# Kernel optimization log

Hardware: AMD Instinct MI355X
Metric: run time of the kernel (lower is better)

Reference implementation:

```python
import jax, jax.numpy as jnp
import numpy as np

NQ = 6; DM = 128; CH = 4; SEQ = 2048; CHUNK = 16; BATCH = 128
NFP = 5 * NQ * 2   # feature params for 2 layers
NMP = 5 * NQ * 2   # mixing params for 2 layers

# ---- batched gate matrices (theta: (B,)) ----

def _rx(t):
    c = jnp.cos(t / 2).astype(jnp.complex64)
    s = (-1j * jnp.sin(t / 2)).astype(jnp.complex64)
    return jnp.stack([jnp.stack([c, s], -1), jnp.stack([s, c], -1)], -2)

def _ry(t):
    c = jnp.cos(t / 2).astype(jnp.complex64)
    s = jnp.sin(t / 2).astype(jnp.complex64)
    return jnp.stack([jnp.stack([c, -s], -1), jnp.stack([s, c], -1)], -2)

def _rz(t):
    e = jnp.exp(-1j * t.astype(jnp.complex64) / 2)
    z = jnp.zeros_like(e)
    return jnp.stack([jnp.stack([e, z], -1), jnp.stack([z, jnp.conj(e)], -1)], -2)

def _crx(t):
    B = t.shape[0]
    r = _rx(t)
    I = jnp.broadcast_to(jnp.eye(2, dtype=jnp.complex64), (B, 2, 2))
    Z = jnp.zeros((B, 2, 2), jnp.complex64)
    return jnp.concatenate([jnp.concatenate([I, Z], -1), jnp.concatenate([Z, r], -1)], -2)

# ---- batched statevector gate application; state: (B, 2, ..., 2) with axis 1+w = wire w ----

def _ap1(s, U, w):
    s = jnp.moveaxis(s, 1 + w, 1)
    sh = s.shape
    s = jnp.einsum('bij,bjr->bir', U, s.reshape(sh[0], 2, -1)).reshape(sh)
    return jnp.moveaxis(s, 1, 1 + w)

def _ap2(s, U, w0, w1):
    s = jnp.moveaxis(s, (1 + w0, 1 + w1), (1, 2))
    sh = s.shape
    s = jnp.einsum('bij,bjr->bir', U, s.reshape(sh[0], 4, -1)).reshape(sh)
    return jnp.moveaxis(s, (1, 2), (1 + w0, 1 + w1))

def _ansatz(s, p, off):
    # RX,RY,RZ on each qubit, then forward CRX ring, then backward CRX ring
    for i in range(NQ):
        s = _ap1(s, _rx(p[:, off + 3 * i]), i)
        s = _ap1(s, _ry(p[:, off + 3 * i + 1]), i)
        s = _ap1(s, _rz(p[:, off + 3 * i + 2]), i)
    off += 3 * NQ
    for i in range(NQ):
        s = _ap2(s, _crx(p[:, off]), i, (i + 1) % NQ)
        off += 1
    for i in range(NQ - 1, -1, -1):
        s = _ap2(s, _crx(p[:, off]), i, (i - 1) % NQ)
        off += 1
    return s, off

def _circuit(angles, fp, mp):
    B = angles.shape[0]
    s = jnp.zeros((B, 2 ** NQ), jnp.complex64).at[:, 0].set(1.0).reshape((B,) + (2,) * NQ)
    for i in range(NQ):                      # RY input embedding
        s = _ap1(s, _ry(angles[:, i]), i)
    off = 0
    for _ in range(2):                        # feature layers
        s, off = _ansatz(s, fp, off)
    off = 0
    for _ in range(2):                        # mixing layers
        s, off = _ansatz(s, mp, off)
    xs, ys, zs = [], [], []
    for i in range(NQ):                       # <X_i>, <Y_i>, <Z_i>
        v = jnp.moveaxis(s, 1 + i, 1).reshape(B, 2, -1)
        a, b = v[:, 0], v[:, 1]
        ab = jnp.sum(jnp.conj(a) * b, -1)
        xs.append(2 * jnp.real(ab))
        ys.append(2 * jnp.imag(ab))
        zs.append(jnp.sum(jnp.abs(a) ** 2 - jnp.abs(b) ** 2, -1))
    return jnp.stack(xs + ys + zs, 1)         # (B, 18) ordered X..Y..Z

def _ln(x, g, b, eps=1e-5):
    m = x.mean(-1, keepdims=True)
    v = ((x - m) ** 2).mean(-1, keepdims=True)
    return (x - m) / jnp.sqrt(v + eps) * g + b

def _fwd(x, conv_w, conv_b, ln1_g, ln1_b, ca1_w, ca1_b, ca2_w, ca2_b, pp_w, pp_b,
         ep_w, ep_b, op_w, op_b, ln2_g, ln2_b, sa1_w, sa1_b, sa2_w, sa2_b,
         cl1_w, cl1_b, cl2_w, cl2_b):
    B, C, S = x.shape
    h = jax.lax.conv_general_dilated(x, conv_w, (1,), [(1, 1)],
                                     dimension_numbers=('NCH', 'OIH', 'NCH')) + conv_b[None, :, None]
    h = jnp.transpose(h, (0, 2, 1))           # (B, S, D)
    h = _ln(h, ln1_g, ln1_b)
    nchunks = S // CHUNK
    h = h.reshape(B * nchunks, CHUNK, DM)
    sc = jnp.tanh(h @ ca1_w + ca1_b) @ ca2_w + ca2_b
    w = jax.nn.softmax(sc, axis=1)
    summ = jnp.sum(w * h, axis=1)             # (B*nchunks, D)
    ap = summ @ pp_w + pp_b
    fp, mp = ap[:, :NFP], ap[:, NFP:]
    ang = jnp.tanh(summ @ ep_w + ep_b) * np.pi
    q = _circuit(ang, fp, mp)                 # (B*nchunks, 18)
    cf = jax.nn.silu(_ln(q @ op_w + op_b, ln2_g, ln2_b))  # dropout = eval identity
    cf = cf.reshape(B, nchunks, DM)
    ss = jnp.tanh(cf @ sa1_w + sa1_b) @ sa2_w + sa2_b
    sw = jax.nn.softmax(ss, axis=1)
    rep = jnp.sum(sw * cf, axis=1)
    return jax.nn.silu(rep @ cl1_w + cl1_b) @ cl2_w + cl2_b

def setup_inputs() -> dict:
    key = jax.random.key(0)
    ks = jax.random.split(key, 16)
    n = lambda k, sh: (jax.random.normal(k, sh, jnp.float32) * 0.05)
    return {
        'x': jax.random.normal(ks[0], (BATCH, CH, SEQ), jnp.float32),
        'conv_w': n(ks[1], (DM, CH, 3)), 'conv_b': jnp.zeros((DM,), jnp.float32),
        'ln1_g': jnp.ones((DM,), jnp.float32), 'ln1_b': jnp.zeros((DM,), jnp.float32),
        'ca1_w': n(ks[2], (DM, DM // 4)), 'ca1_b': jnp.zeros((DM // 4,), jnp.float32),
        'ca2_w': n(ks[3], (DM // 4, 1)), 'ca2_b': jnp.zeros((1,), jnp.float32),
        'pp_w': n(ks[4], (DM, NFP + NMP)), 'pp_b': jnp.zeros((NFP + NMP,), jnp.float32),
        'ep_w': n(ks[5], (DM, NQ)), 'ep_b': jnp.zeros((NQ,), jnp.float32),
        'op_w': n(ks[6], (3 * NQ, DM)), 'op_b': jnp.zeros((DM,), jnp.float32),
        'ln2_g': jnp.ones((DM,), jnp.float32), 'ln2_b': jnp.zeros((DM,), jnp.float32),
        'sa1_w': n(ks[7], (DM, DM // 4)), 'sa1_b': jnp.zeros((DM // 4,), jnp.float32),
        'sa2_w': n(ks[8], (DM // 4, 1)), 'sa2_b': jnp.zeros((1,), jnp.float32),
        'cl1_w': n(ks[9], (DM, DM // 2)), 'cl1_b': jnp.zeros((DM // 2,), jnp.float32),
        'cl2_w': n(ks[10], (DM // 2, 2)), 'cl2_b': jnp.zeros((2,), jnp.float32),
    }

def reference(x, conv_w, conv_b, ln1_g, ln1_b, ca1_w, ca1_b, ca2_w, ca2_b, pp_w, pp_b,
              ep_w, ep_b, op_w, op_b, ln2_g, ln2_b, sa1_w, sa1_b, sa2_w, sa2_b,
              cl1_w, cl1_b, cl2_w, cl2_b):
    return _fwd(x, conv_w, conv_b, ln1_g, ln1_b, ca1_w, ca1_b, ca2_w, ca2_b, pp_w, pp_b,
                ep_w, ep_b, op_w, op_b, ln2_g, ln2_b, sa1_w, sa1_b, sa2_w, sa2_b,
                cl1_w, cl1_b, cl2_w, cl2_b)
```

## Files before the change

kernel.cpp:

```cpp
#include <hip/hip_runtime.h>
#include <math.h>


constexpr int kNQ    = 6;
constexpr int kDM    = 128;
constexpr int kCH    = 4;
constexpr int kSEQ   = 2048;
constexpr int kCHUNK = 16;
constexpr int kBATCH = 128;
constexpr int kNCH   = kSEQ / kCHUNK;
constexpr int kNP    = 120;
constexpr float kPI  = 3.14159265358979323846f;

typedef __attribute__((ext_vector_type(8))) short bf16x8;
typedef __attribute__((ext_vector_type(4))) float f32x4;

__device__ __forceinline__ float fast_tanh(float x) {
  float e = __expf(-2.f * fabsf(x));
  float r = (1.f - e) * __builtin_amdgcn_rcpf(1.f + e);
  return copysignf(r, x);
}
__device__ __forceinline__ float fast_silu(float x) {
  return x * __builtin_amdgcn_rcpf(1.f + __expf(-x));
}

template <int XM>
__device__ __forceinline__ float qp(float v) {
  constexpr int ctrl = (XM == 1) ? 0xB1 : 0x4E;
  return __int_as_float(
      __builtin_amdgcn_update_dpp(0, __float_as_int(v), ctrl, 0xF, 0xF, true));
}


template <int RB>
__device__ __forceinline__ void rx_reg(float c, float s, float* sr, float* si) {
#pragma unroll
  for (int r0 = 0; r0 < 16; ++r0) {
    if (r0 & RB) continue;
    int r1 = r0 | RB;
    float ar = sr[r0], ai = si[r0], br = sr[r1], bi = si[r1];
    sr[r0] = fmaf(c, ar,  s * bi);  si[r0] = fmaf(c, ai, -s * br);
    sr[r1] = fmaf(c, br,  s * ai);  si[r1] = fmaf(c, bi, -s * ar);
  }
}

template <int RB>
__device__ __forceinline__ void ry_reg(float c, float s, float* sr, float* si) {
#pragma unroll
  for (int r0 = 0; r0 < 16; ++r0) {
    if (r0 & RB) continue;
    int r1 = r0 | RB;
    float ar = sr[r0], ai = si[r0], br = sr[r1], bi = si[r1];
    sr[r0] = fmaf(c, ar, -s * br);  si[r0] = fmaf(c, ai, -s * bi);
    sr[r1] = fmaf(s, ar,  c * br);  si[r1] = fmaf(s, ai,  c * bi);
  }
}

template <int RB>
__device__ __forceinline__ void rz_reg(float c, float s, float* sr, float* si) {
#pragma unroll
  for (int r = 0; r < 16; ++r) {
    float sp = (r & RB) ? s : -s;
    float ar = sr[r], ai = si[r];
    sr[r] = fmaf(c, ar, -sp * ai);
    si[r] = fmaf(c, ai,  sp * ar);
  }
}

template <int XM>
__device__ __forceinline__ void rx_lane(float c, float s, float* sr, float* si) {
#pragma unroll
  for (int r = 0; r < 16; ++r) {
    float pr = qp<XM>(sr[r]), pi = qp<XM>(si[r]);
    sr[r] = fmaf(c, sr[r],  s * pi);
    si[r] = fmaf(c, si[r], -s * pr);
  }
}

template <int XM>
__device__ __forceinline__ void ry_lane(float c, float sg, float* sr, float* si) {
#pragma unroll
  for (int r = 0; r < 16; ++r) {
    float pr = qp<XM>(sr[r]), pi = qp<XM>(si[r]);
    sr[r] = fmaf(c, sr[r], sg * pr);
    si[r] = fmaf(c, si[r], sg * pi);
  }
}

__device__ __forceinline__ void rz_lane(float c, float sp, float* sr, float* si) {
#pragma unroll
  for (int r = 0; r < 16; ++r) {
    float ar = sr[r], ai = si[r];
    sr[r] = fmaf(c, ar, -sp * ai);
    si[r] = fmaf(c, ai,  sp * ar);
  }
}

template <int RB, int CB>
__device__ __forceinline__ void crx_reg_reg(float c, float s, float* sr, float* si) {
#pragma unroll
  for (int r0 = 0; r0 < 16; ++r0) {
    if ((r0 & RB) || !(r0 & CB)) continue;
    int r1 = r0 | RB;
    float ar = sr[r0], ai = si[r0], br = sr[r1], bi = si[r1];
    sr[r0] = fmaf(c, ar,  s * bi);  si[r0] = fmaf(c, ai, -s * br);
    sr[r1] = fmaf(c, br,  s * ai);  si[r1] = fmaf(c, bi, -s * ar);
  }
}

template <int XM, int CB>
__device__ __forceinline__ void crx_reg_lane(float c, float s, float* sr, float* si) {
#pragma unroll
  for (int r = 0; r < 16; ++r) {
    if (!(r & CB)) continue;
    float pr = qp<XM>(sr[r]), pi = qp<XM>(si[r]);
    sr[r] = fmaf(c, sr[r],  s * pi);
    si[r] = fmaf(c, si[r], -s * pr);
  }
}

template <int RB>
__device__ __forceinline__ void meas_reg(const float* sr, const float* si,
                                         float& tr, float& ti, float& zz) {
  tr = 0.f; ti = 0.f; zz = 0.f;
#pragma unroll
  for (int r0 = 0; r0 < 16; ++r0) {
    float n = fmaf(sr[r0], sr[r0], si[r0] * si[r0]);
    zz += (r0 & RB) ? -n : n;
    if (r0 & RB) continue;
    int r1 = r0 | RB;
    tr = fmaf(sr[r0], sr[r1], fmaf(si[r0], si[r1], tr));
    ti = fmaf(sr[r0], si[r1], fmaf(-si[r0], sr[r1], ti));
  }
  tr += qp<1>(tr); tr += qp<2>(tr);
  ti += qp<1>(ti); ti += qp<2>(ti);
  zz += qp<1>(zz); zz += qp<2>(zz);
}


__global__ __launch_bounds__(128) void k_pre(
    const float* __restrict__ x,
    const float* __restrict__ conv_w, const float* __restrict__ conv_b,
    const float* __restrict__ ln1_g,  const float* __restrict__ ln1_b,
    const float* __restrict__ ca1_w,  const float* __restrict__ ca1_b,
    const float* __restrict__ ca2_w,  const float* __restrict__ ca2_b,
    const float* __restrict__ pp_w,   const float* __restrict__ pp_b,
    const float* __restrict__ ep_w,   const float* __restrict__ ep_b,
    float* __restrict__ outb, int emit_cs)
{
  __shared__ float hbuf[kCHUNK][132];
  __shared__ __align__(16) float spart[2][16];
  __shared__ __align__(16) float summ[kDM];
  __shared__ float mrow[kCHUNK], irow[kCHUNK];

  const int tid   = threadIdx.x;
  const int chunk = blockIdx.x;
  const int b     = chunk >> 7;
  const int nc    = chunk & 127;
  const int t0    = nc * kCHUNK;
  const int d     = tid;
  const int lane  = tid & 63;
  const int wv    = tid >> 6;
  const int col   = (lane & 15) + 16 * wv;
  const int qd    = lane >> 4;

  float w12[12];
  {
    const float4* cw = (const float4*)(conv_w + d * 12);
    float4 a0 = cw[0], a1 = cw[1], a2 = cw[2];
    w12[0]=a0.x; w12[1]=a0.y; w12[2]=a0.z; w12[3]=a0.w;
    w12[4]=a1.x; w12[5]=a1.y; w12[6]=a1.z; w12[7]=a1.w;
    w12[8]=a2.x; w12[9]=a2.y; w12[10]=a2.z; w12[11]=a2.w;
  }
  float cb = conv_b[d];
  float g1 = ln1_g[d], b1 = ln1_b[d];
  float Bf[32];
#pragma unroll
  for (int ks = 0; ks < 4; ++ks)
#pragma unroll
    for (int jj = 0; jj < 8; ++jj)
      Bf[ks * 8 + jj] = ca1_w[(ks * 32 + qd * 8 + jj) * 32 + col];
  float cb1 = ca1_b[col], cw2 = ca2_w[col], cb2 = ca2_b[0];

  float h[kCHUNK];
#pragma unroll
  for (int t = 0; t < kCHUNK; ++t) h[t] = cb;
#pragma unroll
  for (int ch = 0; ch < kCH; ++ch) {
    const float* xb = x + ((size_t)b * kCH + ch) * kSEQ + t0 - 4;
    float xv[24];
#pragma unroll
    for (int sl = 1; sl <= 4; ++sl) {
      float4 v = *(const float4*)(xb + sl * 4);
      xv[sl*4+0]=v.x; xv[sl*4+1]=v.y; xv[sl*4+2]=v.z; xv[sl*4+3]=v.w;
    }
    if (nc > 0) {
      float4 v = *(const float4*)(xb);
      xv[0]=v.x; xv[1]=v.y; xv[2]=v.z; xv[3]=v.w;
    } else { xv[0]=xv[1]=xv[2]=xv[3]=0.f; }
    if (nc < 127) {
      float4 v = *(const float4*)(xb + 20);
      xv[20]=v.x; xv[21]=v.y; xv[22]=v.z; xv[23]=v.w;
    } else { xv[20]=xv[21]=xv[22]=xv[23]=0.f; }
    float c0 = w12[ch*3+0], c1 = w12[ch*3+1], c2 = w12[ch*3+2];
#pragma unroll
    for (int t = 0; t < kCHUNK; ++t)
      h[t] = fmaf(xv[t+3], c0, fmaf(xv[t+4], c1, fmaf(xv[t+5], c2, h[t])));
  }
#pragma unroll
  for (int t = 0; t < kCHUNK; ++t) hbuf[t][d] = h[t];
  __syncthreads();

  {
    int row = tid >> 3, k = tid & 7;
    const float4* rp = (const float4*)&hbuf[row][k * 16];
    float s1 = 0.f, s2 = 0.f;
#pragma unroll
    for (int q = 0; q < 4; ++q) {
      float4 v = rp[q];
      s1 += v.x + v.y + v.z + v.w;
      s2 = fmaf(v.x,v.x,s2); s2 = fmaf(v.y,v.y,s2);
      s2 = fmaf(v.z,v.z,s2); s2 = fmaf(v.w,v.w,s2);
    }
#pragma unroll
    for (int o = 1; o < 8; o <<= 1) {
      s1 += __shfl_xor(s1, o, 64);
      s2 += __shfl_xor(s2, o, 64);
    }
    if (k == 0) {
      float m = s1 * (1.f / kDM);
      mrow[row] = m;
      irow[row] = rsqrtf(s2 * (1.f / kDM) - m * m + 1e-5f);
    }
  }
  __syncthreads();

#pragma unroll
  for (int t = 0; t < kCHUNK; ++t) {
    h[t] = fmaf((h[t] - mrow[t]) * irow[t], g1, b1);
    unsigned hb = __float_as_uint(h[t]);
    float lof = h[t] - __uint_as_float(hb & 0xffff0000u);
    unsigned pk = (hb >> 16) | (__float_as_uint(lof) & 0xffff0000u);
    ((unsigned*)&hbuf[t][0])[d] = pk;
  }
  __syncthreads();

  bf16x8 bhi[4], blo[4];
#pragma unroll
  for (int ks = 0; ks < 4; ++ks)
#pragma unroll
    for (int jj = 0; jj < 8; ++jj) {
      float bvf = Bf[ks * 8 + jj];
      unsigned bb = __float_as_uint(bvf);
      bhi[ks][jj] = (short)(bb >> 16);
      float lf = bvf - __uint_as_float(bb & 0xffff0000u);
      blo[ks][jj] = (short)(__float_as_uint(lf) >> 16);
    }

  f32x4 acc = {0.f, 0.f, 0.f, 0.f};
  {
    const unsigned* hrow = (const unsigned*)&hbuf[lane & 15][0];
#pragma unroll
    for (int ks = 0; ks < 4; ++ks) {
      const uint4* ap = (const uint4*)(hrow + ks * 32 + qd * 8);
      uint4 w0 = ap[0], w1 = ap[1];
      bf16x8 ahi, alo;
      ahi[0] = (short)(w0.x & 0xffff); ahi[1] = (short)(w0.y & 0xffff);
      ahi[2] = (short)(w0.z & 0xffff); ahi[3] = (short)(w0.w & 0xffff);
      ahi[4] = (short)(w1.x & 0xffff); ahi[5] = (short)(w1.y & 0xffff);
      ahi[6] = (short)(w1.z & 0xffff); ahi[7] = (short)(w1.w & 0xffff);
      alo[0] = (short)(w0.x >> 16); alo[1] = (short)(w0.y >> 16);
      alo[2] = (short)(w0.z >> 16); alo[3] = (short)(w0.w >> 16);
      alo[4] = (short)(w1.x >> 16); alo[5] = (short)(w1.y >> 16);
      alo[6] = (short)(w1.z >> 16); alo[7] = (short)(w1.w >> 16);
      acc = __builtin_amdgcn_mfma_f32_16x16x32_bf16(ahi, bhi[ks], acc, 0, 0, 0);
      acc = __builtin_amdgcn_mfma_f32_16x16x32_bf16(ahi, blo[ks], acc, 0, 0, 0);
      acc = __builtin_amdgcn_mfma_f32_16x16x32_bf16(alo, bhi[ks], acc, 0, 0, 0);
    }
  }

  {
    float ev[4];
#pragma unroll
    for (int r = 0; r < 4; ++r)
      ev[r] = fast_tanh(acc[r] + cb1) * cw2;
#pragma unroll
    for (int o = 1; o < 16; o <<= 1)
#pragma unroll
      for (int r = 0; r < 4; ++r) ev[r] += __shfl_xor(ev[r], o, 64);
    if ((lane & 15) == 0)
      *(float4*)&spart[wv][qd * 4] = make_float4(ev[0], ev[1], ev[2], ev[3]);
  }
  __syncthreads();

  {
    float scl16[kCHUNK];
    const float4* s0 = (const float4*)&spart[0][0];
    const float4* s1 = (const float4*)&spart[1][0];
    float mx = -1e30f;
#pragma unroll
    for (int g = 0; g < 4; ++g) {
      float4 a = s0[g], bq = s1[g];
      scl16[g*4+0] = a.x + bq.x + cb2;
      scl16[g*4+1] = a.y + bq.y + cb2;
      scl16[g*4+2] = a.z + bq.z + cb2;
      scl16[g*4+3] = a.w + bq.w + cb2;
    }
#pragma unroll
    for (int t = 0; t < kCHUNK; ++t) mx = fmaxf(mx, scl16[t]);
    float e[kCHUNK], ssum = 0.f;
#pragma unroll
    for (int t = 0; t < kCHUNK; ++t) { e[t] = __expf(scl16[t] - mx); ssum += e[t]; }
    float inv = 1.f / ssum;
    float acc2 = 0.f;
#pragma unroll
    for (int t = 0; t < kCHUNK; ++t) acc2 = fmaf(e[t] * inv, h[t], acc2);
    summ[d] = acc2;
  }
  __syncthreads();

  if (tid < kNP) {
    float acc = pp_b[tid];
    const float4* s4 = (const float4*)summ;
#pragma unroll 8
    for (int q = 0; q < 32; ++q) {
      float4 v = s4[q];
      acc = fmaf(v.x, pp_w[(q*4+0)*kNP + tid], acc);
      acc = fmaf(v.y, pp_w[(q*4+1)*kNP + tid], acc);
      acc = fmaf(v.z, pp_w[(q*4+2)*kNP + tid], acc);
      acc = fmaf(v.w, pp_w[(q*4+3)*kNP + tid], acc);
    }
    float ha = 0.5f * acc;
    if (emit_cs) {
      ((float2*)(outb + (size_t)chunk * 256))[6 + tid] =
          make_float2(__cosf(ha), __sinf(ha));
    } else {
      outb[(size_t)chunk * 126 + 6 + tid] = ha;
    }
  } else if (tid < kNP + kNQ) {
    int jj = tid - kNP;
    float acc = ep_b[jj];
    const float4* s4 = (const float4*)summ;
#pragma unroll 8
    for (int q = 0; q < 32; ++q) {
      float4 v = s4[q];
      acc = fmaf(v.x, ep_w[(q*4+0)*kNQ + jj], acc);
      acc = fmaf(v.y, ep_w[(q*4+1)*kNQ + jj], acc);
      acc = fmaf(v.z, ep_w[(q*4+2)*kNQ + jj], acc);
      acc = fmaf(v.w, ep_w[(q*4+3)*kNQ + jj], acc);
    }
    float ha = 0.5f * fast_tanh(acc) * kPI;
    if (emit_cs) {
      ((float2*)(outb + (size_t)chunk * 256))[jj] =
          make_float2(__cosf(ha), __sinf(ha));
    } else {
      outb[(size_t)chunk * 126 + jj] = ha;
    }
  }
}


constexpr int kCsStride = 260;

__global__ __launch_bounds__(64) void k_circ_cs(const float* __restrict__ csA,
                                                float* __restrict__ qv_g)
{
  __shared__ __align__(16) float lds[16 * kCsStride];

  const int lane  = threadIdx.x;
  const int c     = lane >> 2;
  const int l     = lane & 3;
  const int chunk = blockIdx.x * 16 + c;
  const int b0 = (l >> 1) & 1;
  const int b1 = l & 1;

  {
    const float4* src = (const float4*)(csA + (size_t)blockIdx.x * 16 * 256);
#pragma unroll
    for (int i = 0; i < 16; ++i) {
      float4 v = src[i * 64 + lane];
      *(float4*)&lds[i * kCsStride + lane * 4] = v;
    }
  }
  __syncthreads();

  const float2* cp = (const float2*)&lds[c * kCsStride];

  float sr[16], si[16];
#pragma unroll
  for (int r = 0; r < 16; ++r) { sr[r] = 0.f; si[r] = 0.f; }
  sr[0] = (l == 0) ? 1.f : 0.f;

  {
    float2 q0 = cp[0], q1 = cp[1], q2 = cp[2], q3 = cp[3], q4 = cp[4], q5 = cp[5];
    ry_lane<2>(q0.x, b0 ? q0.y : -q0.y, sr, si);
    ry_lane<1>(q1.x, b1 ? q1.y : -q1.y, sr, si);
    ry_reg<8>(q2.x, q2.y, sr, si);
    ry_reg<4>(q3.x, q3.y, sr, si);
    ry_reg<2>(q4.x, q4.y, sr, si);
    ry_reg<1>(q5.x, q5.y, sr, si);
  }

  for (int a = 0; a < 4; ++a) {
    const float2* pb = cp + 6 + a * 30;
    float2 t;
    t = pb[0];  rx_lane<2>(t.x, t.y, sr, si);
    t = pb[1];  ry_lane<2>(t.x, b0 ? t.y : -t.y, sr, si);
    t = pb[2];  rz_lane   (t.x, b0 ? t.y : -t.y, sr, si);
    t = pb[3];  rx_lane<1>(t.x, t.y, sr, si);
    t = pb[4];  ry_lane<1>(t.x, b1 ? t.y : -t.y, sr, si);
    t = pb[5];  rz_lane   (t.x, b1 ? t.y : -t.y, sr, si);
    t = pb[6];  rx_reg<8>(t.x, t.y, sr, si);
    t = pb[7];  ry_reg<8>(t.x, t.y, sr, si);
    t = pb[8];  rz_reg<8>(t.x, t.y, sr, si);
    t = pb[9];  rx_reg<4>(t.x, t.y, sr, si);
    t = pb[10]; ry_reg<4>(t.x, t.y, sr, si);
    t = pb[11]; rz_reg<4>(t.x, t.y, sr, si);
    t = pb[12]; rx_reg<2>(t.x, t.y, sr, si);
    t = pb[13]; ry_reg<2>(t.x, t.y, sr, si);
    t = pb[14]; rz_reg<2>(t.x, t.y, sr, si);
    t = pb[15]; rx_reg<1>(t.x, t.y, sr, si);
    t = pb[16]; ry_reg<1>(t.x, t.y, sr, si);
    t = pb[17]; rz_reg<1>(t.x, t.y, sr, si);
    t = pb[18]; { float c2 = b0 ? t.x : 1.f, s2 = b0 ? t.y : 0.f; rx_lane<1>(c2, s2, sr, si); }
    t = pb[19]; { float c2 = b1 ? t.x : 1.f, s2 = b1 ? t.y : 0.f; rx_reg<8>(c2, s2, sr, si); }
    t = pb[20]; crx_reg_reg<4, 8>(t.x, t.y, sr, si);
    t = pb[21]; crx_reg_reg<2, 4>(t.x, t.y, sr, si);
    t = pb[22]; crx_reg_reg<1, 2>(t.x, t.y, sr, si);
    t = pb[23]; crx_reg_lane<2, 1>(t.x, t.y, sr, si);
    t = pb[24]; crx_reg_reg<2, 1>(t.x, t.y, sr, si);
    t = pb[25]; crx_reg_reg<4, 2>(t.x, t.y, sr, si);
    t = pb[26]; crx_reg_reg<8, 4>(t.x, t.y, sr, si);
    t = pb[27]; crx_reg_lane<1, 8>(t.x, t.y, sr, si);
    t = pb[28]; { float c2 = b1 ? t.x : 1.f, s2 = b1 ? t.y : 0.f; rx_lane<2>(c2, s2, sr, si); }
    t = pb[29]; { float c2 = b0 ? t.x : 1.f, s2 = b0 ? t.y : 0.f; rx_reg<1>(c2, s2, sr, si); }
  }

  float res[18];
  {
    float tr = 0.f, ti = 0.f, zz = 0.f;
#pragma unroll
    for (int r = 0; r < 16; ++r) {
      float pr = qp<2>(sr[r]), pi = qp<2>(si[r]);
      tr = fmaf(sr[r], pr, fmaf(si[r], pi, tr));
      ti = fmaf(sr[r], pi, fmaf(-si[r], pr, ti));
      zz = fmaf(sr[r], sr[r], fmaf(si[r], si[r], zz));
    }
    tr = b0 ? 0.f : tr;  ti = b0 ? 0.f : ti;  zz = b0 ? -zz : zz;
    tr += qp<1>(tr); tr += qp<2>(tr);
    ti += qp<1>(ti); ti += qp<2>(ti);
    zz += qp<1>(zz); zz += qp<2>(zz);
    res[0] = 2.f * tr; res[6] = 2.f * ti; res[12] = zz;
  }
  {
    float tr = 0.f, ti = 0.f, zz = 0.f;
#pragma unroll
    for (int r = 0; r < 16; ++r) {
      float pr = qp<1>(sr[r]), pi = qp<1>(si[r]);
      tr = fmaf(sr[r], pr, fmaf(si[r], pi, tr));
      ti = fmaf(sr[r], pi, fmaf(-si[r], pr, ti));
      zz = fmaf(sr[r], sr[r], fmaf(si[r], si[r], zz));
    }
    tr = b1 ? 0.f : tr;  ti = b1 ? 0.f : ti;  zz = b1 ? -zz : zz;
    tr += qp<1>(tr); tr += qp<2>(tr);
    ti += qp<1>(ti); ti += qp<2>(ti);
    zz += qp<1>(zz); zz += qp<2>(zz);
    res[1] = 2.f * tr; res[7] = 2.f * ti; res[13] = zz;
  }
  {
    float tr, ti, zz;
    meas_reg<8>(sr, si, tr, ti, zz); res[2] = 2.f*tr; res[8]  = 2.f*ti; res[14] = zz;
    meas_reg<4>(sr, si, tr, ti, zz); res[3] = 2.f*tr; res[9]  = 2.f*ti; res[15] = zz;
    meas_reg<2>(sr, si, tr, ti, zz); res[4] = 2.f*tr; res[10] = 2.f*ti; res[16] = zz;
    meas_reg<1>(sr, si, tr, ti, zz); res[5] = 2.f*tr; res[11] = 2.f*ti; res[17] = zz;
  }
  if (l == 0) {
    float* qo = qv_g + (size_t)chunk * 18;
#pragma unroll
    for (int k = 0; k < 18; ++k) qo[k] = res[k];
  }
}


__global__ __launch_bounds__(64) void k_circ(const float* __restrict__ csb_g,
                                             float* __restrict__ qv_g)
{
  const int lane  = threadIdx.x;
  const int c     = lane >> 2;
  const int l     = lane & 3;
  const int chunk = blockIdx.x * 16 + c;
  const float* cp = csb_g + (size_t)chunk * 126;
  const int b0 = (l >> 1) & 1;
  const int b1 = l & 1;

  float sr[16], si[16];
#pragma unroll
  for (int r = 0; r < 16; ++r) { sr[r] = 0.f; si[r] = 0.f; }
  sr[0] = (l == 0) ? 1.f : 0.f;

  {
    float gc[6], gs[6];
#pragma unroll
    for (int g = 0; g < 6; ++g) { float th = cp[g]; gc[g] = __cosf(th); gs[g] = __sinf(th); }
    ry_lane<2>(gc[0], b0 ? gs[0] : -gs[0], sr, si);
    ry_lane<1>(gc[1], b1 ? gs[1] : -gs[1], sr, si);
    ry_reg<8>(gc[2], gs[2], sr, si);
    ry_reg<4>(gc[3], gs[3], sr, si);
    ry_reg<2>(gc[4], gs[4], sr, si);
    ry_reg<1>(gc[5], gs[5], sr, si);
// ... 362 lines not shown
    for (int t = 0; t < kCHUNK; ++t) { e[t] = __expf(p[t]-mx); ssum += e[t]; }
    float inv = 1.f/ssum;
    if (tid == 0) {
      float4* w4 = (float4*)wl;
      w4[0]=make_float4(e[0]*inv,e[1]*inv,e[2]*inv,e[3]*inv);
      w4[1]=make_float4(e[4]*inv,e[5]*inv,e[6]*inv,e[7]*inv);
      w4[2]=make_float4(e[8]*inv,e[9]*inv,e[10]*inv,e[11]*inv);
      w4[3]=make_float4(e[12]*inv,e[13]*inv,e[14]*inv,e[15]*inv);
    }
  }
  __syncthreads();
  {
    float acc = 0.f;
    const float4* w4 = (const float4*)wl;
#pragma unroll
    for (int tq = 0; tq < 4; ++tq) {
      float4 wv = w4[tq];
      acc = fmaf(wv.x,hbuf[tq*4+0][d],acc); acc = fmaf(wv.y,hbuf[tq*4+1][d],acc);
      acc = fmaf(wv.z,hbuf[tq*4+2][d],acc); acc = fmaf(wv.w,hbuf[tq*4+3][d],acc);
    }
    summ[d] = acc;
  }
  __syncthreads();
  if (tid < kNP) {
    float acc = pp_b[tid];
    const float4* s4 = (const float4*)summ;
#pragma unroll 8
    for (int q = 0; q < 32; ++q) {
      float4 v = s4[q];
      acc = fmaf(v.x,pp_w[(q*4+0)*kNP+tid],acc); acc = fmaf(v.y,pp_w[(q*4+1)*kNP+tid],acc);
      acc = fmaf(v.z,pp_w[(q*4+2)*kNP+tid],acc); acc = fmaf(v.w,pp_w[(q*4+3)*kNP+tid],acc);
    }
    csb[6+tid] = make_float2(__cosf(0.5f*acc), __sinf(0.5f*acc));
  } else if (tid < kNP + kNQ) {
    int jj = tid - kNP;
    float acc = ep_b[jj];
    for (int dd = 0; dd < kDM; ++dd) acc = fmaf(summ[dd], ep_w[dd*kNQ+jj], acc);
    float a = fast_tanh(acc) * kPI;
    csb[jj] = make_float2(__cosf(0.5f*a), __sinf(0.5f*a));
  }
  float ow[18];
#pragma unroll
  for (int jj = 0; jj < 18; ++jj) ow[jj] = op_w[jj*kDM + d];
  float g2 = ln2_g[d], b2 = ln2_b[d], ob = op_b[d];
  __syncthreads();
  if (tid < 64) {
    int lane = tid;
    float ar = (lane == 0) ? 1.f : 0.f, ai = 0.f;
#pragma unroll
    for (int i = 0; i < kNQ; ++i) fb_ry(csb[i], i, lane, ar, ai);
    fb_ansatz(csb+6, lane, ar, ai);  fb_ansatz(csb+36, lane, ar, ai);
    fb_ansatz(csb+66, lane, ar, ai); fb_ansatz(csb+96, lane, ar, ai);
#pragma unroll
    for (int i = 0; i < kNQ; ++i) {
      int m = 1 << (5-i);
      float pr = __shfl_xor(ar, m, 64), pi = __shfl_xor(ai, m, 64);
      int bit = (lane >> (5-i)) & 1;
      float nrm = fmaf(ar,ar,ai*ai);
      float abr, abi, zz;
      if (bit) { abr = 0.f; abi = 0.f; zz = -nrm; }
      else { abr = fmaf(ar,pr,ai*pi); abi = fmaf(ar,pi,-ai*pr); zz = nrm; }
#pragma unroll
      for (int o = 32; o; o >>= 1) {
        abr += __shfl_xor(abr,o,64); abi += __shfl_xor(abi,o,64); zz += __shfl_xor(zz,o,64);
      }
      if (lane == 0) { qv[i] = 2.f*abr; qv[kNQ+i] = 2.f*abi; qv[2*kNQ+i] = zz; }
    }
  }
  __syncthreads();
  {
    float acc = ob;
#pragma unroll
    for (int jj = 0; jj < 18; ++jj) acc = fmaf(qv[jj], ow[jj], acc);
    float v = acc, v2 = acc*acc;
#pragma unroll
    for (int o = 32; o; o >>= 1) { v += __shfl_xor(v,o,64); v2 += __shfl_xor(v2,o,64); }
    if ((tid & 63) == 0) { red[tid>>6] = v; red[2+(tid>>6)] = v2; }
    __syncthreads();
    float s1 = red[0]+red[1], s2 = red[2]+red[3];
    float m = s1*(1.f/kDM), var = s2*(1.f/kDM) - m*m;
    float xn = fmaf((acc-m)*rsqrtf(var+1e-5f), g2, b2);
    cf[(size_t)chunk*kDM + d] = fast_silu(xn);
  }
}

__global__ __launch_bounds__(256) void k_scl_fb(
    const float* __restrict__ cf,
    const float* __restrict__ sa1_w, const float* __restrict__ sa1_b,
    const float* __restrict__ sa2_w, const float* __restrict__ sa2_b,
    float* __restrict__ scl)
{
  int tid = threadIdx.x, wid = tid >> 6, lane = tid & 63;
  int pair = blockIdx.x * 4 + wid;
  int j = lane & 31, hh = lane >> 5;
  const float4* row = (const float4*)(cf + (size_t)pair*kDM + hh*64);
  const float* wp = sa1_w + (hh*64)*32 + j;
  float acc = 0.f;
#pragma unroll
  for (int q = 0; q < 16; ++q) {
    float4 v = row[q];
    acc = fmaf(v.x,wp[(q*4+0)*32],acc); acc = fmaf(v.y,wp[(q*4+1)*32],acc);
    acc = fmaf(v.z,wp[(q*4+2)*32],acc); acc = fmaf(v.w,wp[(q*4+3)*32],acc);
  }
  acc += __shfl_xor(acc, 32, 64);
  float hv = fast_tanh(acc + sa1_b[j]);
  float v = hv * sa2_w[j];
#pragma unroll
  for (int o = 16; o; o >>= 1) v += __shfl_xor(v, o, 64);
  if (lane == 0) scl[pair] = v + sa2_b[0];
}


extern "C" void kernel_launch(void* const* d_in, const int* in_sizes, int n_in,
                              void* d_out, int out_size, void* d_ws, size_t ws_size,
                              hipStream_t stream) {
  const float* x      = (const float*)d_in[0];
  const float* conv_w = (const float*)d_in[1];
  const float* conv_b = (const float*)d_in[2];
  const float* ln1_g  = (const float*)d_in[3];
  const float* ln1_b  = (const float*)d_in[4];
  const float* ca1_w  = (const float*)d_in[5];
  const float* ca1_b  = (const float*)d_in[6];
  const float* ca2_w  = (const float*)d_in[7];
  const float* ca2_b  = (const float*)d_in[8];
  const float* pp_w   = (const float*)d_in[9];
  const float* pp_b   = (const float*)d_in[10];
  const float* ep_w   = (const float*)d_in[11];
  const float* ep_b   = (const float*)d_in[12];
  const float* op_w   = (const float*)d_in[13];
  const float* op_b   = (const float*)d_in[14];
  const float* ln2_g  = (const float*)d_in[15];
  const float* ln2_b  = (const float*)d_in[16];
  const float* sa1_w  = (const float*)d_in[17];
  const float* sa1_b  = (const float*)d_in[18];
  const float* sa2_w  = (const float*)d_in[19];
  const float* sa2_b  = (const float*)d_in[20];
  const float* cl1_w  = (const float*)d_in[21];
  const float* cl1_b  = (const float*)d_in[22];
  const float* cl2_w  = (const float*)d_in[23];
  const float* cl2_b  = (const float*)d_in[24];
  float* out = (float*)d_out;

  const size_t nch   = (size_t)kBATCH * kNCH;
  const size_t fCS   = nch * 256;
  const size_t need1 = (fCS + nch * 18 + nch) * sizeof(float);
  const size_t fA    = nch * kDM;
  const size_t need2 = (fA + nch * 18 + nch) * sizeof(float);

  if (ws_size >= need1) {
    float* csA   = (float*)d_ws;
    float* cf    = csA;
    float* qv_g  = csA + fCS;
    float* sclb  = qv_g + nch * 18;
    k_pre<<<kBATCH * kNCH, 128, 0, stream>>>(
        x, conv_w, conv_b, ln1_g, ln1_b, ca1_w, ca1_b, ca2_w, ca2_b,
        pp_w, pp_b, ep_w, ep_b, csA, 1);
    k_circ_cs<<<(kBATCH * kNCH) / 16, 64, 0, stream>>>(csA, qv_g);
    k_post<<<kBATCH * kNCH, 128, 0, stream>>>(
        qv_g, op_w, op_b, ln2_g, ln2_b, sa1_w, sa1_b, sa2_w, sa2_b, cf, sclb);
    k_pool_cf<<<kBATCH, 512, 0, stream>>>(
        cf, sclb, cl1_w, cl1_b, cl2_w, cl2_b, out);
  } else if (ws_size >= need2) {
    float* A     = (float*)d_ws;
    float* qv_g  = A + fA;
    float* sclb  = qv_g + nch * 18;
    k_pre<<<kBATCH * kNCH, 128, 0, stream>>>(
        x, conv_w, conv_b, ln1_g, ln1_b, ca1_w, ca1_b, ca2_w, ca2_b,
        pp_w, pp_b, ep_w, ep_b, A, 0);
    k_circ<<<(kBATCH * kNCH) / 16, 64, 0, stream>>>(A, qv_g);
    k_post<<<kBATCH * kNCH, 128, 0, stream>>>(
        qv_g, op_w, op_b, ln2_g, ln2_b, sa1_w, sa1_b, sa2_w, sa2_b, A, sclb);
    k_pool_cf<<<kBATCH, 512, 0, stream>>>(
        A, sclb, cl1_w, cl1_b, cl2_w, cl2_b, out);
  } else {
    float* cf   = (float*)d_ws;
    float* sclb = cf + nch * kDM;
    k_chunk_fb<<<kBATCH * kNCH, 128, 0, stream>>>(
        x, conv_w, conv_b, ln1_g, ln1_b, ca1_w, ca1_b, ca2_w, ca2_b,
        pp_w, pp_b, ep_w, ep_b, op_w, op_b, ln2_g, ln2_b, cf);
    k_scl_fb<<<(kBATCH * kNCH) / 4, 256, 0, stream>>>(cf, sa1_w, sa1_b, sa2_w, sa2_b, sclb);
    k_pool_cf<<<kBATCH, 512, 0, stream>>>(cf, sclb, cl1_w, cl1_b, cl2_w, cl2_b, out);
  }
}
```

Baseline: 225.2 us.

## Process eight chunks per k_pre block to amortize weight loads

```diff
diff --git a/kernel.cpp b/kernel.cpp
--- a/kernel.cpp
+++ b/kernel.cpp
@@ -138,7 +138,7 @@
 }
 
 
-__global__ __launch_bounds__(128) void k_pre(
+__global__ __launch_bounds__(128) void k_pre8(
     const float* __restrict__ x,
     const float* __restrict__ conv_w, const float* __restrict__ conv_b,
     const float* __restrict__ ln1_g,  const float* __restrict__ ln1_b,
@@ -148,21 +148,24 @@
     const float* __restrict__ ep_w,   const float* __restrict__ ep_b,
     float* __restrict__ outb, int emit_cs)
 {
-  __shared__ float hbuf[kCHUNK][132];
+  constexpr int NC = 8;
+
+  __shared__ __align__(16) float xs[kCH][NC * kCHUNK + 4];
+  __shared__ __align__(16) float hbuf[kCHUNK][132];
   __shared__ __align__(16) float spart[2][16];
-  __shared__ __align__(16) float summ[kDM];
+  __shared__ __align__(16) float wl[kCHUNK];
+  __shared__ __align__(16) float sums[NC][kDM];
   __shared__ float mrow[kCHUNK], irow[kCHUNK];
 
-  const int tid   = threadIdx.x;
-  const int chunk = blockIdx.x;
-  const int b     = chunk >> 7;
-  const int nc    = chunk & 127;
-  const int t0    = nc * kCHUNK;
-  const int d     = tid;
-  const int lane  = tid & 63;
-  const int wv    = tid >> 6;
-  const int col   = (lane & 15) + 16 * wv;
-  const int qd    = lane >> 4;
+  const int tid    = threadIdx.x;
+  const int chunk0 = blockIdx.x * NC;
+  const int b      = chunk0 >> 7;
+  const int tloc   = (chunk0 & 127) * kCHUNK;
+  const int d      = tid;
+  const int lane   = tid & 63;
+  const int wv     = tid >> 6;
+  const int col    = (lane & 15) + 16 * wv;
+  const int qd     = lane >> 4;
 
   float w12[12];
   {
@@ -174,187 +177,189 @@
   }
   float cb = conv_b[d];
   float g1 = ln1_g[d], b1 = ln1_b[d];
-  float Bf[32];
+  float cb1 = ca1_b[col], cw2 = ca2_w[col], cb2 = ca2_b[0];
+
+  bf16x8 bhi[4], blo[4];
 #pragma unroll
   for (int ks = 0; ks < 4; ++ks)
 #pragma unroll
-    for (int jj = 0; jj < 8; ++jj)
-      Bf[ks * 8 + jj] = ca1_w[(ks * 32 + qd * 8 + jj) * 32 + col];
-  float cb1 = ca1_b[col], cw2 = ca2_w[col], cb2 = ca2_b[0];
-
-  float h[kCHUNK];
-#pragma unroll
-  for (int t = 0; t < kCHUNK; ++t) h[t] = cb;
-#pragma unroll
-  for (int ch = 0; ch < kCH; ++ch) {
-    const float* xb = x + ((size_t)b * kCH + ch) * kSEQ + t0 - 4;
-    float xv[24];
-#pragma unroll
-    for (int sl = 1; sl <= 4; ++sl) {
-      float4 v = *(const float4*)(xb + sl * 4);
-      xv[sl*4+0]=v.x; xv[sl*4+1]=v.y; xv[sl*4+2]=v.z; xv[sl*4+3]=v.w;
-    }
-    if (nc > 0) {
-      float4 v = *(const float4*)(xb);
-      xv[0]=v.x; xv[1]=v.y; xv[2]=v.z; xv[3]=v.w;
-    } else { xv[0]=xv[1]=xv[2]=xv[3]=0.f; }
-    if (nc < 127) {
-      float4 v = *(const float4*)(xb + 20);
-      xv[20]=v.x; xv[21]=v.y; xv[22]=v.z; xv[23]=v.w;
-    } else { xv[20]=xv[21]=xv[22]=xv[23]=0.f; }
-    float c0 = w12[ch*3+0], c1 = w12[ch*3+1], c2 = w12[ch*3+2];
-#pragma unroll
-    for (int t = 0; t < kCHUNK; ++t)
-      h[t] = fmaf(xv[t+3], c0, fmaf(xv[t+4], c1, fmaf(xv[t+5], c2, h[t])));
-  }
-#pragma unroll
-  for (int t = 0; t < kCHUNK; ++t) hbuf[t][d] = h[t];
-  __syncthreads();
-
-  {
-    int row = tid >> 3, k = tid & 7;
-    const float4* rp = (const float4*)&hbuf[row][k * 16];
-    float s1 = 0.f, s2 = 0.f;
-#pragma unroll
-    for (int q = 0; q < 4; ++q) {
-      float4 v = rp[q];
-      s1 += v.x + v.y + v.z + v.w;
-      s2 = fmaf(v.x,v.x,s2); s2 = fmaf(v.y,v.y,s2);
-      s2 = fmaf(v.z,v.z,s2); s2 = fmaf(v.w,v.w,s2);
-    }
-#pragma unroll
-    for (int o = 1; o < 8; o <<= 1) {
-      s1 += __shfl_xor(s1, o, 64);
-      s2 += __shfl_xor(s2, o, 64);
-    }
-    if (k == 0) {
-      float m = s1 * (1.f / kDM);
-      mrow[row] = m;
-      irow[row] = rsqrtf(s2 * (1.f / kDM) - m * m + 1e-5f);
-    }
-  }
-  __syncthreads();
-
-#pragma unroll
-  for (int t = 0; t < kCHUNK; ++t) {
-    h[t] = fmaf((h[t] - mrow[t]) * irow[t], g1, b1);
-    unsigned hb = __float_as_uint(h[t]);
-    float lof = h[t] - __uint_as_float(hb & 0xffff0000u);
-    unsigned pk = (hb >> 16) | (__float_as_uint(lof) & 0xffff0000u);
-    ((unsigned*)&hbuf[t][0])[d] = pk;
-  }
-  __syncthreads();
-
-  bf16x8 bhi[4], blo[4];
-#pragma unroll
-  for (int ks = 0; ks < 4; ++ks)
-#pragma unroll
     for (int jj = 0; jj < 8; ++jj) {
-      float bvf = Bf[ks * 8 + jj];
+      float bvf = ca1_w[(ks * 32 + qd * 8 + jj) * 32 + col];
       unsigned bb = __float_as_uint(bvf);
       bhi[ks][jj] = (short)(bb >> 16);
       float lf = bvf - __uint_as_float(bb & 0xffff0000u);
       blo[ks][jj] = (short)(__float_as_uint(lf) >> 16);
     }
 
-  f32x4 acc = {0.f, 0.f, 0.f, 0.f};
-  {
-    const unsigned* hrow = (const unsigned*)&hbuf[lane & 15][0];
-#pragma unroll
-    for (int ks = 0; ks < 4; ++ks) {
-      const uint4* ap = (const uint4*)(hrow + ks * 32 + qd * 8);
-      uint4 w0 = ap[0], w1 = ap[1];
-      bf16x8 ahi, alo;
-      ahi[0] = (short)(w0.x & 0xffff); ahi[1] = (short)(w0.y & 0xffff);
-      ahi[2] = (short)(w0.z & 0xffff); ahi[3] = (short)(w0.w & 0xffff);
-      ahi[4] = (short)(w1.x & 0xffff); ahi[5] = (short)(w1.y & 0xffff);
-      ahi[6] = (short)(w1.z & 0xffff); ahi[7] = (short)(w1.w & 0xffff);
-      alo[0] = (short)(w0.x >> 16); alo[1] = (short)(w0.y >> 16);
-      alo[2] = (short)(w0.z >> 16); alo[3] = (short)(w0.w >> 16);
-      alo[4] = (short)(w1.x >> 16); alo[5] = (short)(w1.y >> 16);
-      alo[6] = (short)(w1.z >> 16); alo[7] = (short)(w1.w >> 16);
-      acc = __builtin_amdgcn_mfma_f32_16x16x32_bf16(ahi, bhi[ks], acc, 0, 0, 0);
-      acc = __builtin_amdgcn_mfma_f32_16x16x32_bf16(ahi, blo[ks], acc, 0, 0, 0);
-      acc = __builtin_amdgcn_mfma_f32_16x16x32_bf16(alo, bhi[ks], acc, 0, 0, 0);
-    }
-  }
-
-  {
-    float ev[4];
-#pragma unroll
-    for (int r = 0; r < 4; ++r)
-      ev[r] = fast_tanh(acc[r] + cb1) * cw2;
-#pragma unroll
-    for (int o = 1; o < 16; o <<= 1)
-#pragma unroll
-      for (int r = 0; r < 4; ++r) ev[r] += __shfl_xor(ev[r], o, 64);
-    if ((lane & 15) == 0)
-      *(float4*)&spart[wv][qd * 4] = make_float4(ev[0], ev[1], ev[2], ev[3]);
-  }
-  __syncthreads();
-
-  {
-    float scl16[kCHUNK];
-    const float4* s0 = (const float4*)&spart[0][0];
-    const float4* s1 = (const float4*)&spart[1][0];
-    float mx = -1e30f;
-#pragma unroll
-    for (int g = 0; g < 4; ++g) {
-      float4 a = s0[g], bq = s1[g];
-      scl16[g*4+0] = a.x + bq.x + cb2;
-      scl16[g*4+1] = a.y + bq.y + cb2;
-      scl16[g*4+2] = a.z + bq.z + cb2;
-      scl16[g*4+3] = a.w + bq.w + cb2;
-    }
-#pragma unroll
-    for (int t = 0; t < kCHUNK; ++t) mx = fmaxf(mx, scl16[t]);
-    float e[kCHUNK], ssum = 0.f;
-#pragma unroll
-    for (int t = 0; t < kCHUNK; ++t) { e[t] = __expf(scl16[t] - mx); ssum += e[t]; }
-    float inv = 1.f / ssum;
-    float acc2 = 0.f;
-#pragma unroll
-    for (int t = 0; t < kCHUNK; ++t) acc2 = fmaf(e[t] * inv, h[t], acc2);
-    summ[d] = acc2;
-  }
-  __syncthreads();
-
-  if (tid < kNP) {
-    float acc = pp_b[tid];
-    const float4* s4 = (const float4*)summ;
-#pragma unroll 8
-    for (int q = 0; q < 32; ++q) {
-      float4 v = s4[q];
-      acc = fmaf(v.x, pp_w[(q*4+0)*kNP + tid], acc);
-      acc = fmaf(v.y, pp_w[(q*4+1)*kNP + tid], acc);
-      acc = fmaf(v.z, pp_w[(q*4+2)*kNP + tid], acc);
-      acc = fmaf(v.w, pp_w[(q*4+3)*kNP + tid], acc);
-    }
-    float ha = 0.5f * acc;
-    if (emit_cs) {
-      ((float2*)(outb + (size_t)chunk * 256))[6 + tid] =
-          make_float2(__cosf(ha), __sinf(ha));
-    } else {
-      outb[(size_t)chunk * 126 + 6 + tid] = ha;
-    }
-  } else if (tid < kNP + kNQ) {
-    int jj = tid - kNP;
-    float acc = ep_b[jj];
-    const float4* s4 = (const float4*)summ;
-#pragma unroll 8
-    for (int q = 0; q < 32; ++q) {
-      float4 v = s4[q];
-      acc = fmaf(v.x, ep_w[(q*4+0)*kNQ + jj], acc);
-      acc = fmaf(v.y, ep_w[(q*4+1)*kNQ + jj], acc);
-      acc = fmaf(v.z, ep_w[(q*4+2)*kNQ + jj], acc);
-      acc = fmaf(v.w, ep_w[(q*4+3)*kNQ + jj], acc);
-    }
-    float ha = 0.5f * fast_tanh(acc) * kPI;
-    if (emit_cs) {
-      ((float2*)(outb + (size_t)chunk * 256))[jj] =
-          make_float2(__cosf(ha), __sinf(ha));
-    } else {
-      outb[(size_t)chunk * 126 + jj] = ha;
+#pragma unroll
+  for (int ch = 0; ch < kCH; ++ch) {
+#pragma unroll
+    for (int base = 0; base < 2; ++base) {
+      int pos = base * 128 + tid;
+      if (pos < NC * kCHUNK + 2) {
+        int s = tloc - 1 + pos;
+        float v = 0.f;
+        if (s >= 0 && s < kSEQ) v = x[((size_t)b * kCH + ch) * kSEQ + s];
+        xs[ch][pos] = v;
+      }
+    }
+  }
+  __syncthreads();
+
+  for (int c = 0; c < NC; ++c) {
+    float h[kCHUNK];
+#pragma unroll
+    for (int t = 0; t < kCHUNK; ++t) h[t] = cb;
+#pragma unroll
+    for (int ch = 0; ch < kCH; ++ch) {
+      const float4* xp = (const float4*)&xs[ch][c * kCHUNK];
+      float4 v0 = xp[0], v1 = xp[1], v2 = xp[2], v3 = xp[3], v4 = xp[4];
+      float xr[18];
+      xr[0]=v0.x; xr[1]=v0.y; xr[2]=v0.z; xr[3]=v0.w;
+      xr[4]=v1.x; xr[5]=v1.y; xr[6]=v1.z; xr[7]=v1.w;
+      xr[8]=v2.x; xr[9]=v2.y; xr[10]=v2.z; xr[11]=v2.w;
+      xr[12]=v3.x; xr[13]=v3.y; xr[14]=v3.z; xr[15]=v3.w;
+      xr[16]=v4.x; xr[17]=v4.y;
+      float c0 = w12[ch*3+0], c1 = w12[ch*3+1], c2 = w12[ch*3+2];
+#pragma unroll
+      for (int t = 0; t < kCHUNK; ++t)
+        h[t] = fmaf(xr[t], c0, fmaf(xr[t+1], c1, fmaf(xr[t+2], c2, h[t])));
+    }
+#pragma unroll
+    for (int t = 0; t < kCHUNK; ++t) hbuf[t][d] = h[t];
+    __syncthreads();
+
+    {
+      int row = tid >> 3, k = tid & 7;
+      const float4* rp = (const float4*)&hbuf[row][k * 16];
+      float s1 = 0.f, s2 = 0.f;
+#pragma unroll
+      for (int q = 0; q < 4; ++q) {
+        float4 v = rp[q];
+        s1 += v.x + v.y + v.z + v.w;
+        s2 = fmaf(v.x,v.x,s2); s2 = fmaf(v.y,v.y,s2);
+        s2 = fmaf(v.z,v.z,s2); s2 = fmaf(v.w,v.w,s2);
+      }
+#pragma unroll
+      for (int o = 1; o < 8; o <<= 1) {
+        s1 += __shfl_xor(s1, o, 64);
+        s2 += __shfl_xor(s2, o, 64);
+      }
+      if (k == 0) {
+        float m = s1 * (1.f / kDM);
+        mrow[row] = m;
+        irow[row] = rsqrtf(s2 * (1.f / kDM) - m * m + 1e-5f);
+      }
+    }
+    __syncthreads();
+
+#pragma unroll
+    for (int t = 0; t < kCHUNK; ++t) {
+      h[t] = fmaf((h[t] - mrow[t]) * irow[t], g1, b1);
+      unsigned hb = __float_as_uint(h[t]);
+      float lof = h[t] - __uint_as_float(hb & 0xffff0000u);
+      unsigned pk = (hb >> 16) | (__float_as_uint(lof) & 0xffff0000u);
+      ((unsigned*)&hbuf[t][0])[d] = pk;
+    }
+    __syncthreads();
+
+    f32x4 acc = {0.f, 0.f, 0.f, 0.f};
+    {
+      const unsigned* hrow = (const unsigned*)&hbuf[lane & 15][0];
+#pragma unroll
+      for (int ks = 0; ks < 4; ++ks) {
+        const uint4* ap = (const uint4*)(hrow + ks * 32 + qd * 8);
+        uint4 w0 = ap[0], w1 = ap[1];
+        bf16x8 ahi, alo;
+        ahi[0] = (short)(w0.x & 0xffff); ahi[1] = (short)(w0.y & 0xffff);
+        ahi[2] = (short)(w0.z & 0xffff); ahi[3] = (short)(w0.w & 0xffff);
+        ahi[4] = (short)(w1.x & 0xffff); ahi[5] = (short)(w1.y & 0xffff);
+        ahi[6] = (short)(w1.z & 0xffff); ahi[7] = (short)(w1.w & 0xffff);
+        alo[0] = (short)(w0.x >> 16); alo[1] = (short)(w0.y >> 16);
+        alo[2] = (short)(w0.z >> 16); alo[3] = (short)(w0.w >> 16);
+        alo[4] = (short)(w1.x >> 16); alo[5] = (short)(w1.y >> 16);
+        alo[6] = (short)(w1.z >> 16); alo[7] = (short)(w1.w >> 16);
+        acc = __builtin_amdgcn_mfma_f32_16x16x32_bf16(ahi, bhi[ks], acc, 0, 0, 0);
+        acc = __builtin_amdgcn_mfma_f32_16x16x32_bf16(ahi, blo[ks], acc, 0, 0, 0);
+        acc = __builtin_amdgcn_mfma_f32_16x16x32_bf16(alo, bhi[ks], acc, 0, 0, 0);
+      }
+    }
+
+    {
+      float ev[4];
+#pragma unroll
+      for (int r = 0; r < 4; ++r)
+        ev[r] = fast_tanh(acc[r] + cb1) * cw2;
+#pragma unroll
+      for (int o = 1; o < 16; o <<= 1)
+#pragma unroll
+        for (int r = 0; r < 4; ++r) ev[r] += __shfl_xor(ev[r], o, 64);
+      if ((lane & 15) == 0)
+        *(float4*)&spart[wv][qd * 4] = make_float4(ev[0], ev[1], ev[2], ev[3]);
+    }
+    __syncthreads();
+
+    if (tid < 16) {
+      float scl = spart[0][tid] + spart[1][tid] + cb2;
+      float mx = scl;
+#pragma unroll
+      for (int o = 1; o < 16; o <<= 1) mx = fmaxf(mx, __shfl_xor(mx, o, 64));
+      float e = __expf(scl - mx);
+      float se = e;
+#pragma unroll
+      for (int o = 1; o < 16; o <<= 1) se += __shfl_xor(se, o, 64);
+      wl[tid] = e * (1.f / se);
+    }
+    __syncthreads();
+
+    {
+      const float4* w4 = (const float4*)wl;
+      float4 wa = w4[0], wb = w4[1], wc = w4[2], wd = w4[3];
+      float acc2 = 0.f;
+      acc2 = fmaf(wa.x, h[0],  acc2); acc2 = fmaf(wa.y, h[1],  acc2);
+      acc2 = fmaf(wa.z, h[2],  acc2); acc2 = fmaf(wa.w, h[3],  acc2);
+      acc2 = fmaf(wb.x, h[4],  acc2); acc2 = fmaf(wb.y, h[5],  acc2);
+      acc2 = fmaf(wb.z, h[6],  acc2); acc2 = fmaf(wb.w, h[7],  acc2);
+      acc2 = fmaf(wc.x, h[8],  acc2); acc2 = fmaf(wc.y, h[9],  acc2);
+      acc2 = fmaf(wc.z, h[10], acc2); acc2 = fmaf(wc.w, h[11], acc2);
+      acc2 = fmaf(wd.x, h[12], acc2); acc2 = fmaf(wd.y, h[13], acc2);
+      acc2 = fmaf(wd.z, h[14], acc2); acc2 = fmaf(wd.w, h[15], acc2);
+      sums[c][d] = acc2;
+    }
+  }
+  __syncthreads();
+
+  if (tid < kNP + kNQ) {
+    const bool isep = (tid >= kNP);
+    const int  jj   = tid - kNP;
+    const float* wp = isep ? (ep_w + jj) : (pp_w + tid);
+    const int  ws   = isep ? kNQ : kNP;
+    const int  ws2  = ws * 2, ws3 = ws * 3, ws4 = ws * 4;
+    float bias = isep ? ep_b[jj] : pp_b[tid];
+    float accp[NC];
+#pragma unroll
+    for (int c = 0; c < NC; ++c) accp[c] = bias;
+#pragma unroll 4
+    for (int q4 = 0; q4 < 32; ++q4) {
+      float w0 = wp[0], w1 = wp[ws], w2 = wp[ws2], w3 = wp[ws3];
+      wp += ws4;
+#pragma unroll
+      for (int c = 0; c < NC; ++c) {
+        float4 s = *(const float4*)&sums[c][q4 * 4];
+        accp[c] = fmaf(s.x, w0, fmaf(s.y, w1, fmaf(s.z, w2, fmaf(s.w, w3, accp[c]))));
+      }
+    }
+    const int slot = isep ? jj : (6 + tid);
+#pragma unroll
+    for (int c = 0; c < NC; ++c) {
+      int chunkg = chunk0 + c;
+      float ha = isep ? (0.5f * fast_tanh(accp[c]) * kPI) : (0.5f * accp[c]);
+      if (emit_cs) {
+        ((float2*)(outb + (size_t)chunkg * 256))[slot] =
+            make_float2(__cosf(ha), __sinf(ha));
+      } else {
+        outb[(size_t)chunkg * 126 + slot] = ha;
+      }
     }
   }
 }
@@ -1023,7 +1028,7 @@
     float* cf    = csA;
     float* qv_g  = csA + fCS;
     float* sclb  = qv_g + nch * 18;
-    k_pre<<<kBATCH * kNCH, 128, 0, stream>>>(
+    k_pre8<<<(kBATCH * kNCH) / 8, 128, 0, stream>>>(
         x, conv_w, conv_b, ln1_g, ln1_b, ca1_w, ca1_b, ca2_w, ca2_b,
         pp_w, pp_b, ep_w, ep_b, csA, 1);
     k_circ_cs<<<(kBATCH * kNCH) / 16, 64, 0, stream>>>(csA, qv_g);
@@ -1035,7 +1040,7 @@
     float* A     = (float*)d_ws;
     float* qv_g  = A + fA;
     float* sclb  = qv_g + nch * 18;
-    k_pre<<<kBATCH * kNCH, 128, 0, stream>>>(
+    k_pre8<<<(kBATCH * kNCH) / 8, 128, 0, stream>>>(
         x, conv_w, conv_b, ln1_g, ln1_b, ca1_w, ca1_b, ca2_w, ca2_b,
         pp_w, pp_b, ep_w, ep_b, A, 0);
     k_circ<<<(kBATCH * kNCH) / 16, 64, 0, stream>>>(A, qv_g);
```

After: 208.2 us. -7.5%, faster.
